# Optimization experiments

Hardware: AMD Instinct MI355X
Metric: run time of the kernel (lower is better)

The kernel has to match this reference:

```python
import jax, jax.numpy as jnp
import numpy as np

B, C_IN, H, W = 2, 256, 48, 48
OC, G, KH, KW, PH, PW = 256, 4, 7, 7, 3, 3


def _patches(y, Hn, Wn):
    # y: (B, C, Hp, Wp) -> (B, C, KH, KW, Hn, Wn); stride=1, dilation=1
    return jnp.stack([
        jnp.stack([y[:, :, i:i + Hn, j:j + Wn] for j in range(KW)], axis=2)
        for i in range(KH)
    ], axis=2)


def setup_inputs() -> dict:
    key = jax.random.key(0)
    k1, k2, k3, k4 = jax.random.split(key, 4)
    fan_out = 3 * OC  # 1x1 conv, kaiming fan_out
    conv_w = jax.random.normal(k2, (3 * OC, C_IN), dtype=jnp.float32) * np.sqrt(2.0 / fan_out).astype(np.float32)
    return {
        "x": jax.random.normal(k1, (B, C_IN, H, W), dtype=jnp.float32),
        "conv_w": conv_w,
        "rpe_h": jax.random.normal(k3, (G, 1, KH, 1, (OC // G) // 2), dtype=jnp.float32),
        "rpe_w": jax.random.normal(k4, (G, 1, 1, KW, (OC // G) // 2), dtype=jnp.float32),
    }


def reference(x, conv_w, rpe_h, rpe_w):
    b, c, h, w = x.shape
    goc = OC // G
    c2 = goc // 2
    K = KH * KW
    center = (K - 1) // 2
    ci, cj = center // KW, center % KW

    # 1x1 conv to 3*OC channels, then zero-pad (equiv. to Conv2d(padding) + bias=False)
    y = jnp.einsum('bchw,oc->bohw', x, conv_w)
    y = jnp.pad(y, ((0, 0), (0, 0), (PH, PH), (PW, PW)))
    Hn = h + 2 * PH - (KH - 1)
    Wn = w + 2 * PW - (KW - 1)
    P = Hn * Wn

    q_full, k_full, v_full = jnp.split(y, 3, axis=1)

    # query: only the center element of each window is used
    query = q_full[:, :, ci:ci + Hn, cj:cj + Wn].reshape(b, G, goc, P)
    query = jnp.transpose(query, (0, 1, 3, 2))  # (B,G,P,goc)

    # key: full windows + relative position embeddings
    kp = _patches(k_full, Hn, Wn).reshape(b, G, goc, KH, KW, P)
    key = jnp.transpose(kp, (0, 1, 5, 3, 4, 2))  # (B,G,P,KH,KW,goc)
    key = jnp.concatenate((key[..., :c2] + rpe_h, key[..., c2:] + rpe_w), axis=1)  # (B,2G,P,KH,KW,c2)
    key = key.reshape(b, G, P, K, goc)  # row-major reshape matches torch

    vp = _patches(v_full, Hn, Wn).reshape(b, G, goc, K, P)
    value = jnp.transpose(vp, (0, 1, 4, 3, 2))  # (B,G,P,K,goc)

    att = jax.nn.softmax(jnp.einsum('bgpc,bgpkc->bgpk', query, key), axis=-1)
    out = jnp.einsum('bgpk,bgpkc->bgpc', att, value)  # (B,G,P,goc)
    out = jnp.transpose(out, (0, 1, 3, 2)).reshape(b, OC, Hn, Wn)
    return out
```

## Files before the change

kernel.cpp:

```cpp
#include <hip/hip_runtime.h>

#define BB   2
#define CIN  256
#define OC3  768
#define NG   4
#define GOC  64
#define C2   32
#define KK   49
#define PP   2304
#define HALF_P 1152

#define RS      56
#define BROWS   54
#define BSTRIDE (BROWS * RS * OC3)
#define IOFF    ((3 * RS + 3) * OC3)

#define Y2_BYTES  (BB * BROWS * RS * OC3 * 4)
#define XT_OFF    Y2_BYTES
#define WT_OFF    (XT_OFF + BB * PP * 512 * 2)

typedef __attribute__((ext_vector_type(8))) short bf16x8;
typedef __attribute__((ext_vector_type(4))) float f32x4;

static __device__ __forceinline__ unsigned short f2bf_rne(float x) {
    unsigned int u = __float_as_uint(x);
    unsigned int r = u + 0x7FFFu + ((u >> 16) & 1u);
    return (unsigned short)(r >> 16);
}
static __device__ __forceinline__ float bf2f(unsigned short h) {
    return __uint_as_float(((unsigned int)h) << 16);
}

__global__ __launch_bounds__(256) void convert_w(
    const float* __restrict__ W, short* __restrict__ Wt)
{
    int t = blockIdx.x * 256 + threadIdx.x;
    int o = t >> 8, c = t & 255;
    float v = W[t];
    unsigned short hi = f2bf_rne(v);
    unsigned short lo = f2bf_rne(v - bf2f(hi));
    Wt[(size_t)o * 512 + c]       = (short)hi;
    Wt[(size_t)o * 512 + 256 + c] = (short)lo;
}

__global__ __launch_bounds__(256) void convert_x(
    const float* __restrict__ X, short* __restrict__ Xt)
{
    __shared__ float tile[64][65];
    const int t  = threadIdx.x;
    const int p0 = blockIdx.x * 64;
    const int c0 = blockIdx.y * 64;
    const int b  = blockIdx.z;

    const float* Xb = X + (size_t)b * CIN * PP;
    #pragma unroll
    for (int r = 0; r < 16; ++r) {
        int idx = r * 256 + t;
        int c = idx >> 6, p = idx & 63;
        tile[c][p] = Xb[(size_t)(c0 + c) * PP + p0 + p];
    }
    __syncthreads();
    short* Xo = Xt + (size_t)b * PP * 512;
    #pragma unroll
    for (int r = 0; r < 16; ++r) {
        int idx = r * 256 + t;
        int p = idx >> 6, c = idx & 63;
        float v = tile[c][p];
        unsigned short hi = f2bf_rne(v);
        unsigned short lo = f2bf_rne(v - bf2f(hi));
        size_t base = (size_t)(p0 + p) * 512 + c0 + c;
        Xo[base]       = (short)hi;
        Xo[base + 256] = (short)lo;
    }
}

#define LDA 40

__global__ __launch_bounds__(256, 2) void conv_mfma(
    const short* __restrict__ Wt,
    const short* __restrict__ Xt,
    float* __restrict__ Y2)
{
    __shared__ short As[128 * LDA];
    __shared__ short Bs[128 * LDA];

    const int tid = threadIdx.x;
    const int bn  = blockIdx.x;
    const int bm  = blockIdx.y;
    const int b   = blockIdx.z;
    const int om0 = bm * 128, pn0 = bn * 128;

    const int lane = tid & 63, w = tid >> 6;
    const int oq = (w >> 1) * 64, pq = (w & 1) * 64;
    const int ln15 = lane & 15, q = lane >> 4;

    const int srow = tid >> 1;
    const int soff = (tid & 1) * 16;
    const short* Wg = Wt + (size_t)(om0 + srow) * 512 + soff;
    const short* Xg = Xt + (size_t)b * PP * 512 + (size_t)(pn0 + srow) * 512 + soff;
    short* Asw = &As[srow * LDA + soff];
    short* Bsw = &Bs[srow * LDA + soff];

    f32x4 acc[4][4] = {};

    for (int k0 = 0; k0 < 768; k0 += 32) {
        const int wk = (k0 < 256) ? k0 : k0 - 256;
        const int xk = (k0 < 512) ? k0 : k0 - 512;
        uint4 wa = *(const uint4*)(Wg + wk);
        uint4 wb = *(const uint4*)(Wg + wk + 8);
        uint4 xa = *(const uint4*)(Xg + xk);
        uint4 xb = *(const uint4*)(Xg + xk + 8);
        __syncthreads();
        *(uint4*)(Asw)     = wa;
        *(uint4*)(Asw + 8) = wb;
        *(uint4*)(Bsw)     = xa;
        *(uint4*)(Bsw + 8) = xb;
        __syncthreads();

        bf16x8 af[4], bf[4];
        #pragma unroll
        for (int i = 0; i < 4; ++i) {
            af[i] = *(const bf16x8*)&As[(oq + i * 16 + ln15) * LDA + q * 8];
            bf[i] = *(const bf16x8*)&Bs[(pq + i * 16 + ln15) * LDA + q * 8];
        }
        #pragma unroll
        for (int i = 0; i < 4; ++i)
            #pragma unroll
            for (int j = 0; j < 4; ++j)
                acc[i][j] = __builtin_amdgcn_mfma_f32_16x16x32_bf16(
                    af[i], bf[j], acc[i][j], 0, 0, 0);
    }

    float* Yb = Y2 + (size_t)b * BSTRIDE + IOFF;
    #pragma unroll
    for (int i = 0; i < 4; ++i) {
        #pragma unroll
        for (int j = 0; j < 4; ++j) {
            int o = om0 + oq + i * 16 + q * 4;
            int p = pn0 + pq + j * 16 + ln15;
            int h = p / 48, ww = p - h * 48;
            *(f32x4*)&Yb[(size_t)(h * RS + ww) * OC3 + o] = acc[i][j];
        }
    }
}

struct TagH { static constexpr bool value = true;  };
struct TagW { static constexpr bool value = false; };

__global__ __launch_bounds__(256, 4) void attn_kernel(
    const float* __restrict__ Y2,
    const float* __restrict__ rpe_h,
    const float* __restrict__ rpe_w,
    float* __restrict__ out)
{
    __shared__ float xpose[4][65];

    const int tid  = threadIdx.x;
    const int lane = tid & 63;
    const int w    = tid >> 6;
    const int bx     = blockIdx.x;
    const int wblock = (bx & 7) * 576 + (bx >> 3);
    const int wid    = wblock * 4 + w;
    const int pq   = wid % PP;
    const int g    = (wid / PP) & (NG - 1);
    const int b    = wid / (PP * NG);
    const int ph   = pq / 48;
    const int pw   = pq - ph * 48;

    const float* Yb = Y2 + (size_t)b * BSTRIDE + IOFF;

    const float qv = Yb[(size_t)(ph * RS + pw) * OC3 + g * GOC + lane];

    const int t   = (pq >= HALF_P) ? 1 : 0;
    const int qpr = pq - t * HALF_P;
    const int p0  = 2 * qpr;
    const int ph0 = p0 / 48;
    const int pw0 = p0 - ph0 * 48;
    const int g2  = 2 * g + t;
    const bool use_h = (g2 < NG);
    const int  kch   = use_h ? (CIN + g2 * GOC) : (CIN + (g2 - NG) * GOC + C2);
    const float* rb  = use_h ? (rpe_h + g2 * 7 * C2) : (rpe_w + (g2 - NG) * 7 * C2);

    const int  c  = lane & 31;
    const bool hi = (lane >= 32);

    const float R0 = rb[0 * C2 + c], R1 = rb[1 * C2 + c], R2 = rb[2 * C2 + c],
                R3 = rb[3 * C2 + c], R4 = rb[4 * C2 + c], R5 = rb[5 * C2 + c],
                R6 = rb[6 * C2 + c];

    const float* kb = Yb + (size_t)(ph0 * RS + pw0) * OC3 + kch + c;

    auto rget = [&](int idx) -> float {
        return idx == 0 ? R0 : idx == 1 ? R1 : idx == 2 ? R2 :
               idx == 3 ? R3 : idx == 4 ? R4 : idx == 5 ? R5 : R6;
    };

    auto tree = [&](auto tag) -> float {
        constexpr bool UH = decltype(tag)::value;
        auto chunkprod = [&](int l) -> float {
            int m0 = 2 * l,     h10 = (m0 >= KK), k0 = m0 - KK * h10;
            int m1 = 2 * l + 1, h11 = (m1 >= KK), k1 = m1 - KK * h11;
            int i0 = k0 / 7, j0 = k0 % 7, i1 = k1 / 7, j1 = k1 % 7;
            int d0 = ((i0 - 3) * RS + (h10 + j0 - 3)) * OC3;
            int d1 = ((i1 - 3) * RS + (h11 + j1 - 3)) * OC3;
            float kv = kb[hi ? d1 : d0];
            float ra = UH ? rget(i0) : rget(j0);
            float rc = UH ? rget(i1) : rget(j1);
            kv += hi ? rc : ra;
            return qv * kv;
        };
        float sv[32];
        #pragma unroll
        for (int jj = 0; jj < 32; ++jj) {
            if (2 * jj >= KK) { sv[jj] = 0.f; continue; }
            float pa = chunkprod(2 * jj);
            float pb = (2 * jj + 1 < KK) ? chunkprod(2 * jj + 1) : 0.f;
            float u  = (lane & 1) ? pb : pa;
            float ww = (lane & 1) ? pa : pb;
            sv[jj] = u + __shfl_xor(ww, 1, 64);
        }
        #pragma unroll
        for (int d = 2; d < 64; d <<= 1) {
            #pragma unroll
            for (int i = 0; i < 32; i += d) {
                float a  = sv[i], bb = sv[i + d / 2];
                float u  = (lane & d) ? bb : a;
                float ww = (lane & d) ? a : bb;
                sv[i] = u + __shfl_xor(ww, d, 64);
            }
        }
        return sv[0];
    };

    const float logit = use_h ? tree(TagH{}) : tree(TagW{});

    float mx = logit;
    #pragma unroll
    for (int d = 1; d < 64; d <<= 1)
        mx = fmaxf(mx, __shfl_xor(mx, d, 64));
    float e = (lane < KK) ? __expf(logit - mx) : 0.f;
    float ssum = e;
    #pragma unroll
    for (int d = 1; d < 64; d <<= 1)
        ssum += __shfl_xor(ssum, d, 64);
    const float att = e / ssum;

    float acc = 0.f;
    const float* vb = Yb + (size_t)(ph * RS + pw) * OC3 + 2 * CIN + g * GOC + lane;
    #pragma unroll
    for (int k = 0; k < KK; ++k) {
        int i = k / 7, j = k % 7;
        int doff = ((i - 3) * RS + (j - 3)) * OC3;
        float ak = __uint_as_float(
            __builtin_amdgcn_readlane(__float_as_uint(att), k));
        acc = fmaf(ak, vb[doff], acc);
    }

    xpose[w][lane] = acc;
    __syncthreads();
    const int wid0 = wblock * 4;
    const int pq0  = wid0 % PP;
    const int g0   = (wid0 / PP) & (NG - 1);
    const int b0   = wid0 / (PP * NG);
    const int ch   = tid >> 2;
    const int w2   = tid & 3;
    out[((size_t)b0 * 256 + g0 * GOC + ch) * PP + pq0 + w2] = xpose[w2][ch];
}

extern "C" void kernel_launch(void* const* d_in, const int* in_sizes, int n_in,
                              void* d_out, int out_size, void* d_ws, size_t ws_size,
                              hipStream_t stream)
{
    const float* x  = (const float*)d_in[0];
    const float* w  = (const float*)d_in[1];
    const float* rh = (const float*)d_in[2];
    const float* rw = (const float*)d_in[3];

    float* Y2 = (float*)d_ws;
    short* Xt = (short*)((char*)d_ws + XT_OFF);
    short* Wt = (short*)((char*)d_ws + WT_OFF);

    hipMemsetAsync(d_ws, 0, Y2_BYTES, stream);

    convert_w<<<768, 256, 0, stream>>>(w, Wt);
    convert_x<<<dim3(36, 4, BB), 256, 0, stream>>>(x, Xt);

    conv_mfma<<<dim3(18, 6, BB), 256, 0, stream>>>(Wt, Xt, Y2);

    attn_kernel<<<(BB * NG * PP) / 4, 256, 0, stream>>>(Y2, rh, rw, (float*)d_out);
}
```

Before: 123.6 us.

## Zero only padding border of conv output and shrink GEMM tiles to 64x64

Replaces the full-workspace memset with a kernel that zeroes only the padded border rows and columns of the conv output buffer, since the interior is fully overwritten by the GEMM. The conv GEMM tile shrinks from 128x128 to 64x64 with 2x2 MFMA accumulators per wave, giving four times as many blocks and higher occupancy on the many-CU GPU. In exchange each block reuses less data from LDS and does more global loads per FLOP, and the border-zeroing index maths must exactly cover the padding.

```diff
diff --git a/kernel.cpp b/kernel.cpp
--- a/kernel.cpp
+++ b/kernel.cpp
@@ -31,6 +31,31 @@
     return __uint_as_float(((unsigned int)h) << 16);
 }
 
+#define ROW4  (RS * OC3 / 4)
+#define REG1  (6 * ROW4)
+#define COLS4 (OC3 / 4)
+__global__ __launch_bounds__(256) void zero_guard(float* __restrict__ Y2)
+{
+    const int idx = blockIdx.x * 256 + threadIdx.x;
+    const int b   = blockIdx.y;
+    float4* Yb = (float4*)(Y2 + (size_t)b * BSTRIDE);
+    const float4 z = make_float4(0.f, 0.f, 0.f, 0.f);
+    if (idx < REG1) {
+        int r6  = idx / ROW4;
+        int rem = idx - r6 * ROW4;
+        int r   = (r6 < 3) ? r6 : 48 + r6;
+        Yb[r * ROW4 + rem] = z;
+    } else {
+        int i2  = idx - REG1;
+        int r   = 3 + i2 / (8 * COLS4);
+        int rem = i2 - (r - 3) * (8 * COLS4);
+        int cg  = rem / COLS4;
+        int c   = (cg < 3) ? cg : 48 + cg;
+        int ch4 = rem - cg * COLS4;
+        Yb[(r * RS + c) * COLS4 + ch4] = z;
+    }
+}
+
 __global__ __launch_bounds__(256) void convert_w(
     const float* __restrict__ W, short* __restrict__ Wt)
 {
@@ -76,66 +101,64 @@
 
 #define LDA 40
 
-__global__ __launch_bounds__(256, 2) void conv_mfma(
+__global__ __launch_bounds__(256, 4) void conv_mfma(
     const short* __restrict__ Wt,
     const short* __restrict__ Xt,
     float* __restrict__ Y2)
 {
-    __shared__ short As[128 * LDA];
-    __shared__ short Bs[128 * LDA];
+    __shared__ short As[64 * LDA];
+    __shared__ short Bs[64 * LDA];
 
     const int tid = threadIdx.x;
     const int bn  = blockIdx.x;
     const int bm  = blockIdx.y;
     const int b   = blockIdx.z;
-    const int om0 = bm * 128, pn0 = bn * 128;
+    const int om0 = bm * 64, pn0 = bn * 64;
 
     const int lane = tid & 63, w = tid >> 6;
-    const int oq = (w >> 1) * 64, pq = (w & 1) * 64;
+    const int oq = (w & 1) * 32, pq = (w >> 1) * 32;
     const int ln15 = lane & 15, q = lane >> 4;
 
-    const int srow = tid >> 1;
-    const int soff = (tid & 1) * 16;
-    const short* Wg = Wt + (size_t)(om0 + srow) * 512 + soff;
-    const short* Xg = Xt + (size_t)b * PP * 512 + (size_t)(pn0 + srow) * 512 + soff;
-    short* Asw = &As[srow * LDA + soff];
-    short* Bsw = &Bs[srow * LDA + soff];
-
-    f32x4 acc[4][4] = {};
+    const int  lrow  = (tid & 127) >> 1;
+    const int  lsoff = (tid & 1) * 16;
+    const bool isA   = tid < 128;
+    const short* gA = Wt + (size_t)(om0 + lrow) * 512 + lsoff;
+    const short* gB = Xt + (size_t)b * PP * 512 + (size_t)(pn0 + lrow) * 512 + lsoff;
+    const short* gsrc = isA ? gA : gB;
+    short* ldst = (isA ? As : Bs) + lrow * LDA + lsoff;
+
+    f32x4 acc[2][2] = {};
 
     for (int k0 = 0; k0 < 768; k0 += 32) {
         const int wk = (k0 < 256) ? k0 : k0 - 256;
         const int xk = (k0 < 512) ? k0 : k0 - 512;
-        uint4 wa = *(const uint4*)(Wg + wk);
-        uint4 wb = *(const uint4*)(Wg + wk + 8);
-        uint4 xa = *(const uint4*)(Xg + xk);
-        uint4 xb = *(const uint4*)(Xg + xk + 8);
+        const int kk = isA ? wk : xk;
+        uint4 v0 = *(const uint4*)(gsrc + kk);
+        uint4 v1 = *(const uint4*)(gsrc + kk + 8);
         __syncthreads();
-        *(uint4*)(Asw)     = wa;
-        *(uint4*)(Asw + 8) = wb;
-        *(uint4*)(Bsw)     = xa;
-        *(uint4*)(Bsw + 8) = xb;
+        *(uint4*)ldst       = v0;
+        *(uint4*)(ldst + 8) = v1;
         __syncthreads();
 
-        bf16x8 af[4], bf[4];
-        #pragma unroll
-        for (int i = 0; i < 4; ++i) {
+        bf16x8 af[2], bf[2];
+        #pragma unroll
+        for (int i = 0; i < 2; ++i) {
             af[i] = *(const bf16x8*)&As[(oq + i * 16 + ln15) * LDA + q * 8];
             bf[i] = *(const bf16x8*)&Bs[(pq + i * 16 + ln15) * LDA + q * 8];
         }
         #pragma unroll
-        for (int i = 0; i < 4; ++i)
+        for (int i = 0; i < 2; ++i)
             #pragma unroll
-            for (int j = 0; j < 4; ++j)
+            for (int j = 0; j < 2; ++j)
                 acc[i][j] = __builtin_amdgcn_mfma_f32_16x16x32_bf16(
                     af[i], bf[j], acc[i][j], 0, 0, 0);
     }
 
     float* Yb = Y2 + (size_t)b * BSTRIDE + IOFF;
     #pragma unroll
-    for (int i = 0; i < 4; ++i) {
-        #pragma unroll
-        for (int j = 0; j < 4; ++j) {
+    for (int i = 0; i < 2; ++i) {
+        #pragma unroll
+        for (int j = 0; j < 2; ++j) {
             int o = om0 + oq + i * 16 + q * 4;
             int p = pn0 + pq + j * 16 + ln15;
             int h = p / 48, ww = p - h * 48;
@@ -280,12 +303,11 @@
     short* Xt = (short*)((char*)d_ws + XT_OFF);
     short* Wt = (short*)((char*)d_ws + WT_OFF);
 
-    hipMemsetAsync(d_ws, 0, Y2_BYTES, stream);
-
+    zero_guard<<<dim3(540, BB), 256, 0, stream>>>(Y2);
     convert_w<<<768, 256, 0, stream>>>(w, Wt);
     convert_x<<<dim3(36, 4, BB), 256, 0, stream>>>(x, Xt);
 
-    conv_mfma<<<dim3(18, 6, BB), 256, 0, stream>>>(Wt, Xt, Y2);
+    conv_mfma<<<dim3(36, 12, BB), 256, 0, stream>>>(Wt, Xt, Y2);
 
     attn_kernel<<<(BB * NG * PP) / 4, 256, 0, stream>>>(Y2, rh, rw, (float*)d_out);
 }
```

Measured after the change: 117.4 us. 5.0% less time.
